# Kernel tuning notes

Hardware: AMD Instinct MI355X
Metric: run time of the kernel (lower is better)

Reference implementation:

```python
import jax, jax.numpy as jnp
import numpy as np

NUM_USERS, NUM_ITEMS, DIM = 100000, 50000, 64
BATCH = 1024


def setup_inputs() -> dict:
    key = jax.random.key(0)
    k1, k2, k3, k4, k5, k6 = jax.random.split(key, 6)
    stdv = 1.0 / np.sqrt(DIM)
    return {
        "batch_users": jax.random.randint(k1, (BATCH,), 0, NUM_USERS),
        "whole_items": jnp.arange(NUM_ITEMS),
        "dropout_ration": 0,  # p=0 -> dropout is identity (deterministic reference)
        "user_table": 0.01 * jax.random.normal(k2, (NUM_USERS, DIM), dtype=jnp.float32),
        "item_table": 0.01 * jax.random.normal(k3, (NUM_ITEMS, DIM), dtype=jnp.float32),
        "weight_view": jax.random.uniform(k4, (DIM, 1), minval=-stdv, maxval=stdv, dtype=jnp.float32),
        "weight_cart": jax.random.uniform(k5, (DIM, 1), minval=-stdv, maxval=stdv, dtype=jnp.float32),
        "weight_buy": jax.random.uniform(k6, (DIM, 1), minval=-stdv, maxval=stdv, dtype=jnp.float32),
    }


def reference(batch_users, whole_items, dropout_ration, user_table, item_table,
              weight_view, weight_cart, weight_buy):
    # dropout with p=dropout_ration=0 is the identity
    u = user_table[batch_users]          # [B, D]
    v = item_table[whole_items]          # [I, D]
    # sum_d u[b,d] * v[i,d] * w[d]  ==  (u * w) @ v.T  -- never build [B,I,D]
    def score(w):
        return jnp.einsum('bd,id->bi', u * w[:, 0], v)
    likelihood_view = score(weight_view)
    likelihood_cart = score(weight_cart)
    likelihood_buy = score(weight_buy)
    return likelihood_view, likelihood_cart, likelihood_buy
```

## Files before the change

### kernel.cpp

```cpp
#include <hip/hip_runtime.h>


#define NUM_ITEMS 50000
#define NUM_B     1024
#define DIMK      64
#define ITILE     64
#define UC        32
#define NCHUNK    (NUM_B / UC)
#define VPAD      72

typedef __bf16 bfrag_t __attribute__((ext_vector_type(8)));
typedef float  facc_t  __attribute__((ext_vector_type(4)));

__device__ __forceinline__ unsigned short f2bf(float f) {
    union { float f; unsigned u; } a; a.f = f;
    unsigned r = a.u + 0x7fffu + ((a.u >> 16) & 1u);
    return (unsigned short)(r >> 16);
}

__device__ __forceinline__ bfrag_t cvt8(float4 a, float4 b) {
    bfrag_t r;
    r[0] = (__bf16)a.x; r[1] = (__bf16)a.y; r[2] = (__bf16)a.z; r[3] = (__bf16)a.w;
    r[4] = (__bf16)b.x; r[5] = (__bf16)b.y; r[6] = (__bf16)b.z; r[7] = (__bf16)b.w;
    return r;
}

__global__ __launch_bounds__(256) void gmf_kernel(
    const int*   __restrict__ users,
    const int*   __restrict__ items,
    const float* __restrict__ utab,
    const float* __restrict__ vtab,
    const float* __restrict__ wv,
    const float* __restrict__ wc,
    const float* __restrict__ wb,
    float*       __restrict__ out)
{
    __shared__ unsigned short vt[3][ITILE * VPAD];

    const int t    = threadIdx.x;
    const int wave = t >> 6;
    const int lane = t & 63;
    const int quad = lane >> 4;
    const int l16  = lane & 15;
    const int iblk = blockIdx.x * ITILE;

    #pragma unroll
    for (int c = 0; c < 4; ++c) {
        int idx = t + 256 * c;
        int it  = idx >> 4;
        int f4  = idx & 15;
        int gi  = iblk + it;
        float4 v = make_float4(0.f, 0.f, 0.f, 0.f);
        if (gi < NUM_ITEMS) {
            int row = items[gi];
            v = *(const float4*)(vtab + row * DIMK + f4 * 4);
        }
        float4 w0 = *(const float4*)(wv + f4 * 4);
        float4 w1 = *(const float4*)(wc + f4 * 4);
        float4 w2 = *(const float4*)(wb + f4 * 4);
        ushort4 s;
        s.x = f2bf(v.x * w0.x); s.y = f2bf(v.y * w0.y);
        s.z = f2bf(v.z * w0.z); s.w = f2bf(v.w * w0.w);
        *(ushort4*)(&vt[0][it * VPAD + f4 * 4]) = s;
        s.x = f2bf(v.x * w1.x); s.y = f2bf(v.y * w1.y);
        s.z = f2bf(v.z * w1.z); s.w = f2bf(v.w * w1.w);
        *(ushort4*)(&vt[1][it * VPAD + f4 * 4]) = s;
        s.x = f2bf(v.x * w2.x); s.y = f2bf(v.y * w2.y);
        s.z = f2bf(v.z * w2.z); s.w = f2bf(v.w * w2.w);
        *(ushort4*)(&vt[2][it * VPAD + f4 * 4]) = s;
    }
    __syncthreads();

    bfrag_t vfx[3][2];
    #pragma unroll
    for (int x = 0; x < 3; ++x) {
        const unsigned short* vr = &vt[x][(wave * 16 + l16) * VPAD + quad * 8];
        vfx[x][0] = *(const bfrag_t*)(vr);
        vfx[x][1] = *(const bfrag_t*)(vr + 32);
    }

    const int  icol   = iblk + wave * 16 + quad * 4;
    const bool istore = (icol < NUM_ITEMS);

    float* p[3][2];
    #pragma unroll
    for (int x = 0; x < 3; ++x)
        #pragma unroll
        for (int s = 0; s < 2; ++s)
            p[x][s] = out + ((long)x * NUM_B + s * 16 + l16) * (long)NUM_ITEMS + icol;

    const float* ubase = utab + quad * 8;

    auto loadu = [&](int uc, float4* r) {
        #pragma unroll
        for (int s = 0; s < 2; ++s) {
            int row = users[uc * UC + s * 16 + l16];
            const float* up = ubase + (long)row * DIMK;
            r[s * 4 + 0] = *(const float4*)(up + 0);
            r[s * 4 + 1] = *(const float4*)(up + 4);
            r[s * 4 + 2] = *(const float4*)(up + 32);
            r[s * 4 + 3] = *(const float4*)(up + 36);
        }
    };

    auto compute = [&](const float4* r) {
        bfrag_t a[2][2];
        #pragma unroll
        for (int s = 0; s < 2; ++s) {
            a[s][0] = cvt8(r[s * 4 + 0], r[s * 4 + 1]);
            a[s][1] = cvt8(r[s * 4 + 2], r[s * 4 + 3]);
        }
        facc_t acc[2][3];
        #pragma unroll
        for (int s = 0; s < 2; ++s)
            #pragma unroll
            for (int x = 0; x < 3; ++x)
                acc[s][x] = (facc_t){0.f, 0.f, 0.f, 0.f};
        #pragma unroll
        for (int s = 0; s < 2; ++s)
            #pragma unroll
            for (int x = 0; x < 3; ++x) {
                acc[s][x] = __builtin_amdgcn_mfma_f32_16x16x32_bf16(vfx[x][0], a[s][0], acc[s][x], 0, 0, 0);
                acc[s][x] = __builtin_amdgcn_mfma_f32_16x16x32_bf16(vfx[x][1], a[s][1], acc[s][x], 0, 0, 0);
            }
        if (istore) {
            #pragma unroll
            for (int x = 0; x < 3; ++x)
                #pragma unroll
                for (int s = 0; s < 2; ++s)
                    *(facc_t*)p[x][s] = acc[s][x];
        }
        #pragma unroll
        for (int x = 0; x < 3; ++x)
            #pragma unroll
            for (int s = 0; s < 2; ++s)
                p[x][s] += (long)UC * NUM_ITEMS;
    };

    float4 raw[8];
    loadu(0, raw);
    #pragma unroll 4
    for (int uc = 0; uc < NCHUNK - 1; ++uc) {
        float4 nxt[8];
        loadu(uc + 1, nxt);
        compute(raw);
        #pragma unroll
        for (int i = 0; i < 8; ++i) raw[i] = nxt[i];
    }
    compute(raw);
}

extern "C" void kernel_launch(void* const* d_in, const int* in_sizes, int n_in,
                              void* d_out, int out_size, void* d_ws, size_t ws_size,
                              hipStream_t stream) {
    const int*   users = (const int*)  d_in[0];
    const int*   items = (const int*)  d_in[1];
    const float* utab  = (const float*)d_in[3];
    const float* vtab  = (const float*)d_in[4];
    const float* wv    = (const float*)d_in[5];
    const float* wc    = (const float*)d_in[6];
    const float* wb    = (const float*)d_in[7];
    float* out = (float*)d_out;

    const int grid = (NUM_ITEMS + ITILE - 1) / ITILE;
    gmf_kernel<<<grid, 256, 0, stream>>>(users, items, utab, vtab, wv, wc, wb, out);
}
```

Before: 805.6 us.

## Stage user rows cooperatively through double-buffered LDS and use nontemporal output stores

```diff
diff --git a/kernel.cpp b/kernel.cpp
--- a/kernel.cpp
+++ b/kernel.cpp
@@ -8,6 +8,7 @@
 #define UC        32
 #define NCHUNK    (NUM_B / UC)
 #define VPAD      72
+#define UPAD      72
 
 typedef __bf16 bfrag_t __attribute__((ext_vector_type(8)));
 typedef float  facc_t  __attribute__((ext_vector_type(4)));
@@ -16,13 +17,6 @@
     union { float f; unsigned u; } a; a.f = f;
     unsigned r = a.u + 0x7fffu + ((a.u >> 16) & 1u);
     return (unsigned short)(r >> 16);
-}
-
-__device__ __forceinline__ bfrag_t cvt8(float4 a, float4 b) {
-    bfrag_t r;
-    r[0] = (__bf16)a.x; r[1] = (__bf16)a.y; r[2] = (__bf16)a.z; r[3] = (__bf16)a.w;
-    r[4] = (__bf16)b.x; r[5] = (__bf16)b.y; r[6] = (__bf16)b.z; r[7] = (__bf16)b.w;
-    return r;
 }
 
 __global__ __launch_bounds__(256) void gmf_kernel(
@@ -36,6 +30,7 @@
     float*       __restrict__ out)
 {
     __shared__ unsigned short vt[3][ITILE * VPAD];
+    __shared__ unsigned short ut[2][UC * UPAD];
 
     const int t    = threadIdx.x;
     const int wave = t >> 6;
@@ -44,30 +39,45 @@
     const int l16  = lane & 15;
     const int iblk = blockIdx.x * ITILE;
 
+    const int us = t >> 4;
+    const int f4 = t & 15;
+
     #pragma unroll
     for (int c = 0; c < 4; ++c) {
         int idx = t + 256 * c;
         int it  = idx >> 4;
-        int f4  = idx & 15;
+        int fc  = idx & 15;
         int gi  = iblk + it;
         float4 v = make_float4(0.f, 0.f, 0.f, 0.f);
         if (gi < NUM_ITEMS) {
             int row = items[gi];
-            v = *(const float4*)(vtab + row * DIMK + f4 * 4);
+            v = *(const float4*)(vtab + row * DIMK + fc * 4);
         }
-        float4 w0 = *(const float4*)(wv + f4 * 4);
-        float4 w1 = *(const float4*)(wc + f4 * 4);
-        float4 w2 = *(const float4*)(wb + f4 * 4);
+        float4 w0 = *(const float4*)(wv + fc * 4);
+        float4 w1 = *(const float4*)(wc + fc * 4);
+        float4 w2 = *(const float4*)(wb + fc * 4);
         ushort4 s;
         s.x = f2bf(v.x * w0.x); s.y = f2bf(v.y * w0.y);
         s.z = f2bf(v.z * w0.z); s.w = f2bf(v.w * w0.w);
-        *(ushort4*)(&vt[0][it * VPAD + f4 * 4]) = s;
+        *(ushort4*)(&vt[0][it * VPAD + fc * 4]) = s;
         s.x = f2bf(v.x * w1.x); s.y = f2bf(v.y * w1.y);
         s.z = f2bf(v.z * w1.z); s.w = f2bf(v.w * w1.w);
-        *(ushort4*)(&vt[1][it * VPAD + f4 * 4]) = s;
+        *(ushort4*)(&vt[1][it * VPAD + fc * 4]) = s;
         s.x = f2bf(v.x * w2.x); s.y = f2bf(v.y * w2.y);
         s.z = f2bf(v.z * w2.z); s.w = f2bf(v.w * w2.w);
-        *(ushort4*)(&vt[2][it * VPAD + f4 * 4]) = s;
+        *(ushort4*)(&vt[2][it * VPAD + fc * 4]) = s;
+    }
+
+    {
+        int rowA = users[us];
+        int rowB = users[us + 16];
+        float4 uA = *(const float4*)(utab + (long)rowA * DIMK + f4 * 4);
+        float4 uB = *(const float4*)(utab + (long)rowB * DIMK + f4 * 4);
+        ushort4 s;
+        s.x = f2bf(uA.x); s.y = f2bf(uA.y); s.z = f2bf(uA.z); s.w = f2bf(uA.w);
+        *(ushort4*)(&ut[0][us * UPAD + f4 * 4]) = s;
+        s.x = f2bf(uB.x); s.y = f2bf(uB.y); s.z = f2bf(uB.z); s.w = f2bf(uB.w);
+        *(ushort4*)(&ut[0][(us + 16) * UPAD + f4 * 4]) = s;
     }
     __syncthreads();
 
@@ -89,65 +99,65 @@
         for (int s = 0; s < 2; ++s)
             p[x][s] = out + ((long)x * NUM_B + s * 16 + l16) * (long)NUM_ITEMS + icol;
 
-    const float* ubase = utab + quad * 8;
+    #pragma unroll 2
+    for (int uc = 0; uc < NCHUNK; ++uc) {
+        const int cb = uc & 1;
 
-    auto loadu = [&](int uc, float4* r) {
+        float4 uA, uB;
+        if (uc + 1 < NCHUNK) {
+            int rowA = users[(uc + 1) * UC + us];
+            int rowB = users[(uc + 1) * UC + us + 16];
+            uA = *(const float4*)(utab + (long)rowA * DIMK + f4 * 4);
+            uB = *(const float4*)(utab + (long)rowB * DIMK + f4 * 4);
+        }
+
+        bfrag_t b[2][2];
         #pragma unroll
         for (int s = 0; s < 2; ++s) {
-            int row = users[uc * UC + s * 16 + l16];
-            const float* up = ubase + (long)row * DIMK;
-            r[s * 4 + 0] = *(const float4*)(up + 0);
-            r[s * 4 + 1] = *(const float4*)(up + 4);
-            r[s * 4 + 2] = *(const float4*)(up + 32);
-            r[s * 4 + 3] = *(const float4*)(up + 36);
+            const unsigned short* ur = &ut[cb][(s * 16 + l16) * UPAD + quad * 8];
+            b[s][0] = *(const bfrag_t*)(ur);
+            b[s][1] = *(const bfrag_t*)(ur + 32);
         }
-    };
 
-    auto compute = [&](const float4* r) {
-        bfrag_t a[2][2];
-        #pragma unroll
-        for (int s = 0; s < 2; ++s) {
-            a[s][0] = cvt8(r[s * 4 + 0], r[s * 4 + 1]);
-            a[s][1] = cvt8(r[s * 4 + 2], r[s * 4 + 3]);
-        }
         facc_t acc[2][3];
         #pragma unroll
         for (int s = 0; s < 2; ++s)
             #pragma unroll
             for (int x = 0; x < 3; ++x)
                 acc[s][x] = (facc_t){0.f, 0.f, 0.f, 0.f};
+
         #pragma unroll
         for (int s = 0; s < 2; ++s)
             #pragma unroll
             for (int x = 0; x < 3; ++x) {
-                acc[s][x] = __builtin_amdgcn_mfma_f32_16x16x32_bf16(vfx[x][0], a[s][0], acc[s][x], 0, 0, 0);
-                acc[s][x] = __builtin_amdgcn_mfma_f32_16x16x32_bf16(vfx[x][1], a[s][1], acc[s][x], 0, 0, 0);
+                acc[s][x] = __builtin_amdgcn_mfma_f32_16x16x32_bf16(vfx[x][0], b[s][0], acc[s][x], 0, 0, 0);
+                acc[s][x] = __builtin_amdgcn_mfma_f32_16x16x32_bf16(vfx[x][1], b[s][1], acc[s][x], 0, 0, 0);
             }
+
         if (istore) {
             #pragma unroll
             for (int x = 0; x < 3; ++x)
                 #pragma unroll
                 for (int s = 0; s < 2; ++s)
-                    *(facc_t*)p[x][s] = acc[s][x];
+                    __builtin_nontemporal_store(acc[s][x], (facc_t*)p[x][s]);
         }
         #pragma unroll
         for (int x = 0; x < 3; ++x)
             #pragma unroll
             for (int s = 0; s < 2; ++s)
                 p[x][s] += (long)UC * NUM_ITEMS;
-    };
 
-    float4 raw[8];
-    loadu(0, raw);
-    #pragma unroll 4
-    for (int uc = 0; uc < NCHUNK - 1; ++uc) {
-        float4 nxt[8];
-        loadu(uc + 1, nxt);
-        compute(raw);
-        #pragma unroll
-        for (int i = 0; i < 8; ++i) raw[i] = nxt[i];
+        if (uc + 1 < NCHUNK) {
+            ushort4 s;
+            s.x = f2bf(uA.x); s.y = f2bf(uA.y); s.z = f2bf(uA.z); s.w = f2bf(uA.w);
+            *(ushort4*)(&ut[cb ^ 1][us * UPAD + f4 * 4]) = s;
+            s.x = f2bf(uB.x); s.y = f2bf(uB.y); s.z = f2bf(uB.z); s.w = f2bf(uB.w);
+            *(ushort4*)(&ut[cb ^ 1][(us + 16) * UPAD + f4 * 4]) = s;
+
+            asm volatile("s_waitcnt lgkmcnt(0)" ::: "memory");
+            __builtin_amdgcn_s_barrier();
+        }
     }
-    compute(raw);
 }
 
 extern "C" void kernel_launch(void* const* d_in, const int* in_sizes, int n_in,
```

Result: faster. 704.0 us (-12.6%).
